# Performance work log

Measured on AMD Instinct MI355X. Metric: run time of the kernel, lower is better.

The kernel has to match this reference:

```python
import jax, jax.numpy as jnp
import numpy as np

BN_EPS = 1e-5

def conv1x1(x, w, b):
    # x: [B,C,H,W], w: [O,C], b: [O]
    return jnp.einsum('bchw,oc->bohw', x, w) + b[None, :, None, None]

def maxpool2x2(x):
    B, C, H, W = x.shape
    return x.reshape(B, C, H // 2, 2, W // 2, 2).max(axis=(3, 5))

def setup_inputs() -> dict:
    key = jax.random.key(0)
    ks = jax.random.split(key, 11)
    B, C, H, W = 8, 256, 64, 64
    Ci = C // 2  # inter_channels = 128
    s_in = 1.0 / np.sqrt(C)
    s_int = 1.0 / np.sqrt(Ci)
    return {
        'x': jax.random.normal(ks[0], (B, C, H, W), jnp.float32),
        'theta_w': jax.random.uniform(ks[1], (Ci, C), jnp.float32, -s_in, s_in),
        'theta_b': jax.random.uniform(ks[2], (Ci,), jnp.float32, -s_in, s_in),
        'phi_w': jax.random.uniform(ks[3], (Ci, C), jnp.float32, -s_in, s_in),
        'phi_b': jax.random.uniform(ks[4], (Ci,), jnp.float32, -s_in, s_in),
        'g_w': jax.random.uniform(ks[5], (Ci, C), jnp.float32, -s_in, s_in),
        'g_b': jax.random.uniform(ks[6], (Ci,), jnp.float32, -s_in, s_in),
        'W_w': jax.random.uniform(ks[7], (C, Ci), jnp.float32, -s_int, s_int),
        'W_b': jax.random.uniform(ks[8], (C,), jnp.float32, -s_int, s_int),
        'bn_gamma': jax.random.normal(ks[9], (C,), jnp.float32) * 0.1 + 1.0,
        'bn_beta': jax.random.normal(ks[10], (C,), jnp.float32) * 0.1,
    }

def reference(x, theta_w, theta_b, phi_w, phi_b, g_w, g_b, W_w, W_b, bn_gamma, bn_beta):
    B, C, H, W = x.shape
    Ci = theta_w.shape[0]
    # g and phi are sub-sampled (2x2 maxpool) after the 1x1 conv
    g_x = maxpool2x2(conv1x1(x, g_w, g_b)).reshape(B, Ci, -1)        # [B,Ci,M]
    g_x = g_x.transpose(0, 2, 1)                                     # [B,M,Ci]
    theta_x = conv1x1(x, theta_w, theta_b).reshape(B, Ci, -1)        # [B,Ci,N]
    theta_x = theta_x.transpose(0, 2, 1)                             # [B,N,Ci]
    phi_x = maxpool2x2(conv1x1(x, phi_w, phi_b)).reshape(B, Ci, -1)  # [B,Ci,M]
    f = jnp.einsum('bnc,bcm->bnm', theta_x, phi_x)                   # [B,N,M]
    f_div_C = jax.nn.softmax(f, axis=-1)
    y = jnp.einsum('bnm,bmc->bnc', f_div_C, g_x)                     # [B,N,Ci]
    y = y.transpose(0, 2, 1).reshape(B, Ci, H, W)
    # 1x1 conv + BatchNorm2d (training-mode batch statistics)
    W_y = conv1x1(y, W_w, W_b)
    mean = W_y.mean(axis=(0, 2, 3))
    var = W_y.var(axis=(0, 2, 3))
    W_y = (W_y - mean[None, :, None, None]) * jax.lax.rsqrt(var + BN_EPS)[None, :, None, None]
    W_y = W_y * bn_gamma[None, :, None, None] + bn_beta[None, :, None, None]
    return W_y + x
```

## Files before the change

kernel.cpp:

```cpp
#include <hip/hip_runtime.h>
#include <hip/hip_bf16.h>
#include <cstdint>
#include <math.h>

using bf16 = __hip_bfloat16;
typedef __attribute__((ext_vector_type(8))) short bf16x8;
typedef __attribute__((ext_vector_type(4))) float f32x4;

#define DEV __device__ __forceinline__

DEV float b2f(unsigned short u) { return __uint_as_float(((uint32_t)u) << 16); }
DEV float bfl(bf16 h) { return __bfloat162float(h); }
DEV short f2bs(float f) { bf16 h = __float2bfloat16(f); return *(short*)&h; }
DEV float ldv(const void* p, int isbf, int i) {
  return isbf ? bfl(((const bf16*)p)[i]) : ((const float*)p)[i];
}

DEV bf16x8 load_wfrag(const void* w, int isbf, int row, int K, int off) {
  bf16x8 r;
  if (isbf) {
    r = *(const bf16x8*)((const short*)w + (size_t)row * K + off);
  } else {
    const float* f = (const float*)w + (size_t)row * K + off;
    float4 a = *(const float4*)f, b = *(const float4*)(f + 4);
    r[0] = f2bs(a.x); r[1] = f2bs(a.y); r[2] = f2bs(a.z); r[3] = f2bs(a.w);
    r[4] = f2bs(b.x); r[5] = f2bs(b.y); r[6] = f2bs(b.z); r[7] = f2bs(b.w);
  }
  return r;
}

__global__ __launch_bounds__(256) void sniff_kernel(
    const unsigned short* __restrict__ xr, int* __restrict__ flag)
{
  int tid = threadIdx.x;
  int good = 0;
  for (int k = tid; k < 16384; k += 256) {
    unsigned short u = xr[2 * k];
    int e = (u >> 7) & 0xFF;
    good += (e >= 0x6A && e <= 0x86) ? 1 : 0;
  }
  __shared__ int r[256];
  r[tid] = good;
  __syncthreads();
  for (int off = 128; off; off >>= 1) {
    if (tid < off) r[tid] += r[tid + off];
    __syncthreads();
  }
  if (tid == 0) *flag = (r[0] > 9830) ? 1 : 0;
}

__global__ __launch_bounds__(256) void transpose_x(
    const void* __restrict__ x, short* __restrict__ xT, const int* __restrict__ flag)
{
  const int isbf = *flag;
  __shared__ short lt[64 * 71];
  const int n0 = blockIdx.x * 64, c0 = blockIdx.y * 64, b = blockIdx.z;
  const int tid = threadIdx.x;
  for (int it = 0; it < 4; ++it) {
    int idx4 = it * 256 + tid;
    int ci = idx4 >> 4, n4 = (idx4 & 15) * 4;
    size_t go = ((size_t)(b * 256 + c0 + ci)) * 4096 + n0 + n4;
    if (isbf) {
      ushort4 v = *(const ushort4*)((const unsigned short*)x + go);
      lt[ci * 71 + n4 + 0] = v.x; lt[ci * 71 + n4 + 1] = v.y;
      lt[ci * 71 + n4 + 2] = v.z; lt[ci * 71 + n4 + 3] = v.w;
    } else {
      float4 v = *(const float4*)((const float*)x + go);
      lt[ci * 71 + n4 + 0] = f2bs(v.x); lt[ci * 71 + n4 + 1] = f2bs(v.y);
      lt[ci * 71 + n4 + 2] = f2bs(v.z); lt[ci * 71 + n4 + 3] = f2bs(v.w);
    }
  }
  __syncthreads();
  for (int it = 0; it < 4; ++it) {
    int idx4 = it * 256 + tid;
    int n = idx4 >> 4, c4 = (idx4 & 15) * 4;
    ushort4 v;
    v.x = (unsigned short)lt[(c4 + 0) * 71 + n];
    v.y = (unsigned short)lt[(c4 + 1) * 71 + n];
    v.z = (unsigned short)lt[(c4 + 2) * 71 + n];
    v.w = (unsigned short)lt[(c4 + 3) * 71 + n];
    *(ushort4*)(xT + ((size_t)(b * 4096 + n0 + n)) * 256 + c0 + c4) = v;
  }
}

__global__ __launch_bounds__(256) void conv_t_k(
    const short* __restrict__ xT, const void* __restrict__ w,
    const void* __restrict__ bias, short* __restrict__ out,
    const int* __restrict__ flag)
{
  const int isbf = *flag;
  __shared__ short sh[64 * 264];
  const int b = blockIdx.y, nbase = blockIdx.x * 64, tid = threadIdx.x;
  const int ln = tid & 15, q = (tid >> 4) & 3, wv = tid >> 6;
  for (int it = 0; it < 16; ++it) {
    int idx4 = it * 256 + tid;
    int n = idx4 >> 6, c4 = (idx4 & 63) * 4;
    *(ushort4*)&sh[n * 264 + c4] =
        *(const ushort4*)(xT + ((size_t)(b * 4096 + nbase + n)) * 256 + c4);
  }
  __syncthreads();
  f32x4 zero = {0.f, 0.f, 0.f, 0.f};
  f32x4 acc[4][2];
  for (int nt = 0; nt < 4; ++nt) for (int ti = 0; ti < 2; ++ti) acc[nt][ti] = zero;

  for (int kk = 0; kk < 8; ++kk) {
    int off = kk * 32 + q * 8;
    bf16x8 a[4];
    #pragma unroll
    for (int nt = 0; nt < 4; ++nt)
      a[nt] = *(const bf16x8*)&sh[(16 * nt + ln) * 264 + off];
    #pragma unroll
    for (int ti = 0; ti < 2; ++ti) {
      bf16x8 bw = load_wfrag(w, isbf, 16 * (2 * wv + ti) + ln, 256, off);
      #pragma unroll
      for (int nt = 0; nt < 4; ++nt)
        acc[nt][ti] = __builtin_amdgcn_mfma_f32_16x16x32_bf16(a[nt], bw, acc[nt][ti], 0, 0, 0);
    }
  }
  __syncthreads();
  float bv[2];
  for (int ti = 0; ti < 2; ++ti) bv[ti] = ldv(bias, isbf, 16 * (2 * wv + ti) + ln);
  for (int nt = 0; nt < 4; ++nt)
    for (int ti = 0; ti < 2; ++ti)
      for (int r = 0; r < 4; ++r)
        sh[(16 * nt + q * 4 + r) * 136 + 16 * (2 * wv + ti) + ln] =
            f2bs(acc[nt][ti][r] + bv[ti]);
  __syncthreads();
  for (int it = 0; it < 8; ++it) {
    int idx4 = it * 256 + tid;
    int n = idx4 >> 5, c4 = (idx4 & 31) * 4;
    *(ushort4*)(out + ((size_t)(b * 4096 + nbase + n)) * 128 + c4) =
        *(const ushort4*)&sh[n * 136 + c4];
  }
}

template<int CO, int K>
__global__ __launch_bounds__(256) void conv_n_k(
    const short* __restrict__ inp, const void* __restrict__ w,
    const void* __restrict__ bias, short* __restrict__ out,
    const int* __restrict__ flag)
{
  const int isbf = *flag;
  constexpr int XS = 64 * (K + 8);
  constexpr int OS = CO * 68;
  __shared__ short sh[(XS > OS ? XS : OS)];
  const int b = blockIdx.y, nbase = blockIdx.x * 64, tid = threadIdx.x;
  const int ln = tid & 15, q = (tid >> 4) & 3, wv = tid >> 6;
  constexpr int TPW = CO / 64;
  constexpr int KS = (K == 256) ? 6 : 5;
  for (int it = 0; it < 64 * K / 1024; ++it) {
    int idx4 = it * 256 + tid;
    int n = idx4 >> KS, c4 = (idx4 & ((K / 4) - 1)) * 4;
    *(ushort4*)&sh[n * (K + 8) + c4] =
        *(const ushort4*)(inp + ((size_t)(b * 4096 + nbase + n)) * K + c4);
  }
  __syncthreads();
  f32x4 zero = {0.f, 0.f, 0.f, 0.f};
  f32x4 acc[TPW][4];
  for (int ti = 0; ti < TPW; ++ti) for (int nt = 0; nt < 4; ++nt) acc[ti][nt] = zero;

  for (int kk = 0; kk < K / 32; ++kk) {
    int off = kk * 32 + q * 8;
    bf16x8 bx[4];
    #pragma unroll
    for (int nt = 0; nt < 4; ++nt)
      bx[nt] = *(const bf16x8*)&sh[(16 * nt + ln) * (K + 8) + off];
    #pragma unroll
    for (int ti = 0; ti < TPW; ++ti) {
      bf16x8 aw = load_wfrag(w, isbf, 16 * (TPW * wv + ti) + ln, K, off);
      #pragma unroll
      for (int nt = 0; nt < 4; ++nt)
        acc[ti][nt] = __builtin_amdgcn_mfma_f32_16x16x32_bf16(aw, bx[nt], acc[ti][nt], 0, 0, 0);
    }
  }
  __syncthreads();
  for (int ti = 0; ti < TPW; ++ti)
    for (int r = 0; r < 4; ++r) {
      int co = 16 * (TPW * wv + ti) + q * 4 + r;
      float bb = ldv(bias, isbf, co);
      for (int nt = 0; nt < 4; ++nt)
        sh[co * 68 + 16 * nt + ln] = f2bs(acc[ti][nt][r] + bb);
    }
  __syncthreads();
  for (int it = 0; it < 64 * CO / 1024; ++it) {
    int idx4 = it * 256 + tid;
    int co = idx4 >> 4, n4 = (idx4 & 15) * 4;
    *(ushort4*)(out + ((size_t)(b * CO + co)) * 4096 + nbase + n4) =
        *(const ushort4*)&sh[co * 68 + n4];
  }
}

__global__ __launch_bounds__(256) void pool_phi_kernel(
    const short* __restrict__ pc, short* __restrict__ phi)
{
  int idx = blockIdx.x * 256 + threadIdx.x;
  int ci = idx & 127, m = (idx >> 7) & 1023, b = idx >> 17;
  int mh = m >> 5, mw = m & 31;
  const short* p = pc + ((size_t)(b * 4096 + (mh * 2) * 64 + mw * 2)) * 128 + ci;
  float v = fmaxf(fmaxf(b2f(p[0]), b2f(p[128])),
                  fmaxf(b2f(p[64 * 128]), b2f(p[65 * 128])));
  phi[idx] = f2bs(v);
}

__global__ __launch_bounds__(256) void pool_g_kernel(
    const short* __restrict__ gc, short* __restrict__ g)
{
  int idx = blockIdx.x * 256 + threadIdx.x;
  int m = idx & 1023, bc = idx >> 10;
  int mh = m >> 5, mw = m & 31;
  const short* p = gc + (size_t)bc * 4096 + mh * 128 + mw * 2;
  float v = fmaxf(fmaxf(b2f(p[0]), b2f(p[1])), fmaxf(b2f(p[64]), b2f(p[65])));
  g[idx] = f2bs(v);
}

__global__ __launch_bounds__(256) void attn_kernel(
    const short* __restrict__ theta, const short* __restrict__ phi,
    const short* __restrict__ g, short* __restrict__ y)
{
  __shared__ short th[64 * 136];
  __shared__ short ph[64 * 136];
  __shared__ short gl[128 * 72];
  __shared__ short Pl[64 * 72];
  const int b = blockIdx.y, nbase = blockIdx.x * 64, tid = threadIdx.x;
  const int ln = tid & 15, q = (tid >> 4) & 3, wv = tid >> 6;

  for (int it = 0; it < 8; ++it) {
    int idx4 = it * 256 + tid;
    int n = idx4 >> 5, c4 = (idx4 & 31) * 4;
    *(ushort4*)&th[n * 136 + c4] =
        *(const ushort4*)(theta + ((size_t)(b * 4096 + nbase + n)) * 128 + c4);
  }

  f32x4 zero = {0.f, 0.f, 0.f, 0.f};
  f32x4 yacc[8], lacc = zero;
  for (int t = 0; t < 8; ++t) yacc[t] = zero;
  bf16x8 ones;
  #pragma unroll
  for (int j = 0; j < 8; ++j) ones[j] = 0x3F80;

  for (int mc = 0; mc < 16; ++mc) {
    __syncthreads();
    for (int it = 0; it < 8; ++it) {
      int idx4 = it * 256 + tid;
      int m = idx4 >> 5, c4 = (idx4 & 31) * 4;
      *(ushort4*)&ph[m * 136 + c4] =
          *(const ushort4*)(phi + ((size_t)(b * 1024 + mc * 64 + m)) * 128 + c4);
    }
    for (int it = 0; it < 8; ++it) {
      int idx4 = it * 256 + tid;
      int ci = idx4 >> 4, m4 = (idx4 & 15) * 4;
      *(ushort4*)&gl[ci * 72 + m4] =
          *(const ushort4*)(g + ((size_t)(b * 128 + ci)) * 1024 + mc * 64 + m4);
    }
    __syncthreads();

    bf16x8 a[4];
    #pragma unroll
    for (int kk = 0; kk < 4; ++kk)
      a[kk] = *(const bf16x8*)&th[(16 * wv + ln) * 136 + kk * 32 + q * 8];
    #pragma unroll
    for (int t = 0; t < 4; ++t) {
      f32x4 s = zero;
      #pragma unroll
      for (int kk = 0; kk < 4; ++kk) {
        bf16x8 bp = *(const bf16x8*)&ph[(16 * t + ln) * 136 + kk * 32 + q * 8];
        s = __builtin_amdgcn_mfma_f32_16x16x32_bf16(a[kk], bp, s, 0, 0, 0);
      }
      #pragma unroll
      for (int r = 0; r < 4; ++r)
        Pl[(16 * wv + q * 4 + r) * 72 + 16 * t + ln] =
            f2bs(__expf(fminf(s[r], 80.f)));
    }
    bf16x8 ap[2];
    #pragma unroll
    for (int kk = 0; kk < 2; ++kk)
      ap[kk] = *(const bf16x8*)&Pl[(16 * wv + ln) * 72 + kk * 32 + q * 8];
    #pragma unroll
    for (int kk = 0; kk < 2; ++kk)
      lacc = __builtin_amdgcn_mfma_f32_16x16x32_bf16(ap[kk], ones, lacc, 0, 0, 0);
    #pragma unroll
    for (int t = 0; t < 8; ++t) {
      #pragma unroll
      for (int kk = 0; kk < 2; ++kk) {
        bf16x8 bg = *(const bf16x8*)&gl[(16 * t + ln) * 72 + kk * 32 + q * 8];
        yacc[t] = __builtin_amdgcn_mfma_f32_16x16x32_bf16(ap[kk], bg, yacc[t], 0, 0, 0);
      }
    }
  }
  __syncthreads();

  float li[4];
  #pragma unroll
  for (int r = 0; r < 4; ++r) li[r] = 1.0f / lacc[r];
  for (int t = 0; t < 8; ++t)
    for (int r = 0; r < 4; ++r)
      ph[(16 * wv + q * 4 + r) * 136 + 16 * t + ln] = f2bs(yacc[t][r] * li[r]);
  __syncthreads();
  for (int it = 0; it < 8; ++it) {
    int idx4 = it * 256 + tid;
    int n = idx4 >> 5, c4 = (idx4 & 31) * 4;
    *(ushort4*)(y + ((size_t)(b * 4096 + nbase + n)) * 128 + c4) =
        *(const ushort4*)&ph[n * 136 + c4];
  }
}

__global__ __launch_bounds__(256) void bn_stats_kernel(
    const short* __restrict__ Wy, const void* __restrict__ gamma,
    const void* __restrict__ beta, float* __restrict__ stats,
    const int* __restrict__ flag)
{
  const int isbf = *flag;
  const int c = blockIdx.x;
  const int tid = threadIdx.x;
  float s = 0.f, s2 = 0.f;
  for (int b = 0; b < 8; ++b) {
    const short* p = Wy + ((size_t)(b * 256 + c)) * 4096;
    for (int i = tid; i < 4096; i += 256) {
      float v = b2f(p[i]);
      s += v; s2 += v * v;
    }
  }
  __shared__ float rs[256], rs2[256];
  rs[tid] = s; rs2[tid] = s2;
  __syncthreads();
  for (int off = 128; off > 0; off >>= 1) {
    if (tid < off) { rs[tid] += rs[tid + off]; rs2[tid] += rs2[tid + off]; }
    __syncthreads();
  }
  if (tid == 0) {
    float mean = rs[0] * (1.0f / 32768.0f);
    float var = rs2[0] * (1.0f / 32768.0f) - mean * mean;
    var = fmaxf(var, 0.f);
    float rstd = rsqrtf(var + 1e-5f);
    float scale = rstd * ldv(gamma, isbf, c);
    stats[c] = scale;
    stats[256 + c] = ldv(beta, isbf, c) - mean * scale;
  }
}

__global__ __launch_bounds__(256) void bn_apply_kernel(
    const short* __restrict__ Wy, const void* __restrict__ x,
    const float* __restrict__ stats, void* __restrict__ out,
    const int* __restrict__ flag)
{
  const int isbf = *flag;
  int idx = blockIdx.x * 256 + threadIdx.x;
  int c = (idx >> 12) & 255;
  float xv = isbf ? bfl(((const bf16*)x)[idx]) : ((const float*)x)[idx];
  float v = b2f(Wy[idx]) * stats[c] + stats[256 + c] + xv;
  if (isbf) ((bf16*)out)[idx] = __float2bfloat16(v);
  else      ((float*)out)[idx] = v;
}

extern "C" void kernel_launch(void* const* d_in, const int* in_sizes, int n_in,
                              void* d_out, int out_size, void* d_ws, size_t ws_size,
                              hipStream_t stream) {
  const void* x       = d_in[0];
  const void* theta_w = d_in[1];
  const void* theta_b = d_in[2];
  const void* phi_w   = d_in[3];
  const void* phi_b   = d_in[4];
  const void* g_w     = d_in[5];
  const void* g_b     = d_in[6];
  const void* W_w     = d_in[7];
  const void* W_b     = d_in[8];
  const void* gamma   = d_in[9];
  const void* beta    = d_in[10];

  char* wsb = (char*)d_ws;
  short* xT      = (short*)(wsb + 0);
  short* ybuf    = (short*)(wsb + 0);
  short* theta   = (short*)(wsb + 16777216);
  short* W_y     = (short*)(wsb + 16777216);
  short* scratch = (short*)(wsb + 25165824);
  short* phi     = (short*)(wsb + 33554432);
  short* gg      = (short*)(wsb + 35651584);
  float* stats   = (float*)(wsb + 37748736);
  int*   flag    = (int*)  (wsb + 37750784);

  dim3 blk(256);
  dim3 cgrid(64, 8);
  dim3 tgrid(64, 4, 8);

  sniff_kernel<<<1, blk, 0, stream>>>((const unsigned short*)x, flag);
  transpose_x<<<tgrid, blk, 0, stream>>>(x, xT, flag);
  conv_t_k<<<cgrid, blk, 0, stream>>>(xT, theta_w, theta_b, theta, flag);
  conv_t_k<<<cgrid, blk, 0, stream>>>(xT, phi_w, phi_b, scratch, flag);
  pool_phi_kernel<<<4096, blk, 0, stream>>>(scratch, phi);
  conv_n_k<128, 256><<<cgrid, blk, 0, stream>>>(xT, g_w, g_b, scratch, flag);
  pool_g_kernel<<<4096, blk, 0, stream>>>(scratch, gg);
  attn_kernel<<<cgrid, blk, 0, stream>>>(theta, phi, gg, ybuf);
  conv_n_k<256, 128><<<cgrid, blk, 0, stream>>>(ybuf, W_w, W_b, W_y, flag);
  bn_stats_kernel<<<256, blk, 0, stream>>>(W_y, gamma, beta, stats, flag);
  bn_apply_kernel<<<32768, blk, 0, stream>>>(W_y, x, stats, d_out, flag);
}
```

Baseline: 265.7 us.

## Fuse BN statistics into W conv epilogue and vectorize BN apply

```diff
diff --git a/kernel.cpp b/kernel.cpp
--- a/kernel.cpp
+++ b/kernel.cpp
@@ -12,6 +12,10 @@
 DEV float b2f(unsigned short u) { return __uint_as_float(((uint32_t)u) << 16); }
 DEV float bfl(bf16 h) { return __bfloat162float(h); }
 DEV short f2bs(float f) { bf16 h = __float2bfloat16(f); return *(short*)&h; }
+DEV uint32_t pk2(float a, float b) {
+  return (uint32_t)(unsigned short)f2bs(a) |
+         ((uint32_t)(unsigned short)f2bs(b) << 16);
+}
 DEV float ldv(const void* p, int isbf, int i) {
   return isbf ? bfl(((const bf16*)p)[i]) : ((const float*)p)[i];
 }
@@ -304,52 +308,107 @@
   }
 }
 
-__global__ __launch_bounds__(256) void bn_stats_kernel(
-    const short* __restrict__ Wy, const void* __restrict__ gamma,
-    const void* __restrict__ beta, float* __restrict__ stats,
+__global__ __launch_bounds__(256, 4) void convW_k(
+    const short* __restrict__ yb, const void* __restrict__ w,
+    const void* __restrict__ bias, short* __restrict__ Wy,
+    float* __restrict__ stats, const int* __restrict__ flag)
+{
+  const int isbf = *flag;
+  __shared__ short sh[256 * 72];
+  const int b = blockIdx.y, nbase = blockIdx.x * 64, tid = threadIdx.x;
+  const int ln = tid & 15, q = (tid >> 4) & 3, wv = tid >> 6;
+
+  for (int it = 0; it < 4; ++it) {
+    int idx8 = it * 256 + tid;
+    int n = idx8 >> 4, c8 = (idx8 & 15) * 8;
+    *(uint4*)&sh[n * 136 + c8] =
+        *(const uint4*)(yb + ((size_t)(b * 4096 + nbase + n)) * 128 + c8);
+  }
+  __syncthreads();
+  f32x4 zero = {0.f, 0.f, 0.f, 0.f};
+  f32x4 acc[4][4];
+  for (int ti = 0; ti < 4; ++ti)
+    for (int nt = 0; nt < 4; ++nt) acc[ti][nt] = zero;
+
+  for (int kk = 0; kk < 4; ++kk) {
+    int off = kk * 32 + q * 8;
+    bf16x8 bx[4];
+    #pragma unroll
+    for (int nt = 0; nt < 4; ++nt)
+      bx[nt] = *(const bf16x8*)&sh[(16 * nt + ln) * 136 + off];
+    #pragma unroll
+    for (int ti = 0; ti < 4; ++ti) {
+      bf16x8 aw = load_wfrag(w, isbf, 16 * (4 * wv + ti) + ln, 128, off);
+      #pragma unroll
+      for (int nt = 0; nt < 4; ++nt)
+        acc[ti][nt] = __builtin_amdgcn_mfma_f32_16x16x32_bf16(aw, bx[nt], acc[ti][nt], 0, 0, 0);
+    }
+  }
+  __syncthreads();
+  #pragma unroll
+  for (int ti = 0; ti < 4; ++ti)
+    #pragma unroll
+    for (int r = 0; r < 4; ++r) {
+      int co = 16 * (4 * wv + ti) + 4 * q + r;
+      float bb = ldv(bias, isbf, co);
+      #pragma unroll
+      for (int nt = 0; nt < 4; ++nt)
+        sh[co * 72 + 16 * nt + ln] = f2bs(acc[ti][nt][r] + bb);
+    }
+  __syncthreads();
+  {
+    int co = tid;
+    float s = 0.f, s2 = 0.f;
+    for (int i = 0; i < 64; ++i) {
+      float v = b2f((unsigned short)sh[co * 72 + i]);
+      s += v; s2 += v * v;
+    }
+    atomicAdd(&stats[co], s);
+    atomicAdd(&stats[256 + co], s2);
+  }
+  for (int it = 0; it < 8; ++it) {
+    int idx8 = it * 256 + tid;
+    int co = idx8 >> 3, n8 = (idx8 & 7) * 8;
+    *(uint4*)(Wy + ((size_t)(b * 256 + co)) * 4096 + nbase + n8) =
+        *(const uint4*)&sh[co * 72 + n8];
+  }
+}
+
+__global__ __launch_bounds__(256) void bn_apply4(
+    const short* __restrict__ Wy, const void* __restrict__ x,
+    const float* __restrict__ stats, const void* __restrict__ gamma,
+    const void* __restrict__ beta, void* __restrict__ out,
     const int* __restrict__ flag)
 {
   const int isbf = *flag;
-  const int c = blockIdx.x;
-  const int tid = threadIdx.x;
-  float s = 0.f, s2 = 0.f;
-  for (int b = 0; b < 8; ++b) {
-    const short* p = Wy + ((size_t)(b * 256 + c)) * 4096;
-    for (int i = tid; i < 4096; i += 256) {
-      float v = b2f(p[i]);
-      s += v; s2 += v * v;
-    }
-  }
-  __shared__ float rs[256], rs2[256];
-  rs[tid] = s; rs2[tid] = s2;
-  __syncthreads();
-  for (int off = 128; off > 0; off >>= 1) {
-    if (tid < off) { rs[tid] += rs[tid + off]; rs2[tid] += rs2[tid + off]; }
-    __syncthreads();
-  }
-  if (tid == 0) {
-    float mean = rs[0] * (1.0f / 32768.0f);
-    float var = rs2[0] * (1.0f / 32768.0f) - mean * mean;
-    var = fmaxf(var, 0.f);
-    float rstd = rsqrtf(var + 1e-5f);
-    float scale = rstd * ldv(gamma, isbf, c);
-    stats[c] = scale;
-    stats[256 + c] = ldv(beta, isbf, c) - mean * scale;
-  }
-}
-
-__global__ __launch_bounds__(256) void bn_apply_kernel(
-    const short* __restrict__ Wy, const void* __restrict__ x,
-    const float* __restrict__ stats, void* __restrict__ out,
-    const int* __restrict__ flag)
-{
-  const int isbf = *flag;
-  int idx = blockIdx.x * 256 + threadIdx.x;
-  int c = (idx >> 12) & 255;
-  float xv = isbf ? bfl(((const bf16*)x)[idx]) : ((const float*)x)[idx];
-  float v = b2f(Wy[idx]) * stats[c] + stats[256 + c] + xv;
-  if (isbf) ((bf16*)out)[idx] = __float2bfloat16(v);
-  else      ((float*)out)[idx] = v;
+  int t = blockIdx.x * 256 + threadIdx.x;
+  int idx4 = t * 4;
+  int c = (idx4 >> 12) & 255;
+  float s = stats[c], s2 = stats[256 + c];
+  float mean = s * (1.0f / 32768.0f);
+  float var = fmaxf(s2 * (1.0f / 32768.0f) - mean * mean, 0.f);
+  float scale = rsqrtf(var + 1e-5f) * ldv(gamma, isbf, c);
+  float shift = ldv(beta, isbf, c) - mean * scale;
+  ushort4 wy = *(const ushort4*)(Wy + idx4);
+  float xv[4];
+  if (isbf) {
+    ushort4 xu = *(const ushort4*)((const unsigned short*)x + idx4);
+    xv[0] = b2f(xu.x); xv[1] = b2f(xu.y); xv[2] = b2f(xu.z); xv[3] = b2f(xu.w);
+  } else {
+    float4 xf = *(const float4*)((const float*)x + idx4);
+    xv[0] = xf.x; xv[1] = xf.y; xv[2] = xf.z; xv[3] = xf.w;
+  }
+  float v0 = b2f(wy.x) * scale + shift + xv[0];
+  float v1 = b2f(wy.y) * scale + shift + xv[1];
+  float v2 = b2f(wy.z) * scale + shift + xv[2];
+  float v3 = b2f(wy.w) * scale + shift + xv[3];
+  if (isbf) {
+    uint2 o; o.x = pk2(v0, v1); o.y = pk2(v2, v3);
+    *(uint2*)((unsigned short*)out + idx4) = o;
+  } else {
+    float4 o = make_float4(v0, v1, v2, v3);
+    *(float4*)((float*)out + idx4) = o;
+  }
 }
 
 extern "C" void kernel_launch(void* const* d_in, const int* in_sizes, int n_in,
@@ -382,6 +441,7 @@
   dim3 cgrid(64, 8);
   dim3 tgrid(64, 4, 8);
 
+  hipMemsetAsync(stats, 0, 2048, stream);
   sniff_kernel<<<1, blk, 0, stream>>>((const unsigned short*)x, flag);
   transpose_x<<<tgrid, blk, 0, stream>>>(x, xT, flag);
   conv_t_k<<<cgrid, blk, 0, stream>>>(xT, theta_w, theta_b, theta, flag);
@@ -390,7 +450,6 @@
   conv_n_k<128, 256><<<cgrid, blk, 0, stream>>>(xT, g_w, g_b, scratch, flag);
   pool_g_kernel<<<4096, blk, 0, stream>>>(scratch, gg);
   attn_kernel<<<cgrid, blk, 0, stream>>>(theta, phi, gg, ybuf);
-  conv_n_k<256, 128><<<cgrid, blk, 0, stream>>>(ybuf, W_w, W_b, W_y, flag);
-  bn_stats_kernel<<<256, blk, 0, stream>>>(W_y, gamma, beta, stats, flag);
-  bn_apply_kernel<<<32768, blk, 0, stream>>>(W_y, x, stats, d_out, flag);
-}
+  convW_k<<<cgrid, blk, 0, stream>>>(ybuf, W_w, W_b, W_y, stats, flag);
+  bn_apply4<<<8192, blk, 0, stream>>>(W_y, x, stats, gamma, beta, d_out, flag);
+}
```

Result: faster. 241.0 us (-9.3%).
